# Kernel optimization log

Hardware: AMD Instinct MI355X
Metric: run time of the kernel (lower is better)

The kernel has to match this reference:

```python
import jax, jax.numpy as jnp
import numpy as np

H, W = 256, 256           # image_size
RES = 8                   # resolution
LAM_NOOBJ, LAM_ACCEL, LAM_VEL = 0.5, 1.0, 1.0
B_IMG = 129               # number of unique image indices in train_labels
K_BOX = 64                # boxes per image


def _make_labels():
    """Build label rows: [x, y, w, h, vx, vy, ax, ay, flag, img_idx] (int32).
    Cells are distinct within each image so scatter order is irrelevant."""
    rng = np.random.default_rng(0)
    rows = []
    for i in range(B_IMG):
        cells = rng.choice(H * W, K_BOX, replace=False)
        yc, xc = cells // W, cells % W
        x = xc * RES + rng.integers(0, RES, K_BOX)
        y = yc * RES + rng.integers(0, RES, K_BOX)
        wh = rng.integers(1, 32, (K_BOX, 2))
        traj = rng.integers(-10, 11, (K_BOX, 4))
        flag = np.full((K_BOX, 1), -1 if i % 16 == 0 else 0)
        img = np.full((K_BOX, 1), i)
        rows.append(np.concatenate([x[:, None], y[:, None], wh, traj, flag, img], axis=1))
    return np.concatenate(rows, 0).astype(np.int32)


def setup_inputs() -> dict:
    key = jax.random.key(0)
    output = jax.random.normal(key, (B_IMG - 1, 5, H, W), dtype=jnp.float32)
    train_labels = jnp.asarray(_make_labels())
    return {"output": output, "train_labels": train_labels, "num_images": B_IMG}


def _transform(train_labels, num_images):
    """Vectorized transform_LSTM_train: scatter per-box trajectories into dense grids."""
    Bm1 = num_images - 1
    img = train_labels[:, -1]
    # flag of each image's first row (constant per image in the data)
    first_flag = jax.ops.segment_max(train_labels[:, -2], img, num_segments=num_images)
    # loop starts at image 1; images whose flag == -1 are skipped
    valid = (img >= 1) & (first_flag[img] != -1)
    xc = train_labels[:, 0] // RES
    yc = train_labels[:, 1] // RES
    traj_v = train_labels[:, 4:8].astype(jnp.float32)
    # route invalid rows into an extra padding slot, then slice it off
    b = jnp.where(valid, img - 1, Bm1)
    traj = jnp.zeros((Bm1 + 1, 4, H, W), jnp.float32).at[b, :, yc, xc].set(traj_v)[:Bm1]
    o_m = jnp.zeros((Bm1 + 1, 1, H, W), jnp.float32).at[b, 0, yc, xc].set(1.0)[:Bm1]
    return traj, o_m


def _loss(output, traj, o_m):
    obj = o_m > 0           # [Bm1,1,H,W], broadcasts over channel dim
    noobj = ~obj
    pred_vel, pred_accel, pred_obj = output[:, :2], output[:, 2:4], output[:, -1:]
    n_obj = jnp.sum(obj).astype(jnp.float32)
    n_noobj = jnp.sum(noobj).astype(jnp.float32)
    # F.mse_loss over boolean-masked selections == masked sum / count
    noobj_loss = jnp.sum(jnp.where(noobj, (pred_obj - o_m) ** 2, 0.0)) / jnp.maximum(n_noobj, 1.0)
    vel_loss = jnp.sum(jnp.where(obj, (pred_vel - traj[:, :2]) ** 2, 0.0)) / jnp.maximum(2.0 * n_obj, 1.0)
    accel_loss = jnp.sum(jnp.where(obj, (pred_accel - traj[:, 2:]) ** 2, 0.0)) / jnp.maximum(2.0 * n_obj, 1.0)
    full = LAM_NOOBJ * noobj_loss + LAM_VEL * vel_loss + LAM_ACCEL * accel_loss
    return jnp.where(n_obj == 0, LAM_NOOBJ * noobj_loss, full)


def reference(output, train_labels, num_images):
    traj, o_m = _transform(train_labels, num_images)
    return _loss(output, traj, o_m)
```

## Files before the change

### kernel.cpp

```cpp
#include <hip/hip_runtime.h>
#include <limits.h>

constexpr int HW = 65536;
constexpr int RES_SHIFT = 3;
constexpr int NB = 1024;
constexpr int TPB = 256;

__device__ inline float wave_sum(float v) {
#pragma unroll
    for (int o = 32; o > 0; o >>= 1) v += __shfl_down(v, o, 64);
    return v;
}


__global__ void k_main(const float* __restrict__ out, int total4,
                       const int* __restrict__ labels, int n_rows,
                       float* __restrict__ partials_all,
                       float4* __restrict__ box_p) {
    const int nbox = (n_rows + TPB - 1) / TPB;
    const bool boxblk = blockIdx.x < nbox;

    bool bvalid = false;
    float o0 = 0, o1 = 0, o2 = 0, o3 = 0, o4 = 0;
    float vx = 0, vy = 0, ax = 0, ay = 0;
    if (boxblk) {
        int r = blockIdx.x * TPB + threadIdx.x;
        bool inb = r < n_rows;
        int flag = INT_MIN, img = -7, x = 0, y = 0;
        if (inb) {
            const int* L = labels + (size_t)r * 10;
            x = L[0]; y = L[1];
            vx = (float)L[4]; vy = (float)L[5];
            ax = (float)L[6]; ay = (float)L[7];
            flag = L[8]; img = L[9];
        }
        int f = flag;
#pragma unroll
        for (int o = 1; o < 64; o <<= 1) {
            int of = __shfl_xor(f, o, 64);
            int ok = __shfl_xor(img, o, 64);
            if (ok == img) f = max(f, of);
        }
        if (inb && img >= 1 && f != -1) {
            bvalid = true;
            int b = img - 1;
            int xc = x >> RES_SHIFT;
            int yc = y >> RES_SHIFT;
            size_t base = (((size_t)(b * 5)) << 16) + ((size_t)yc << 8) + (size_t)xc;
            o0 = out[base];
            o1 = out[base + HW];
            o2 = out[base + 2 * (size_t)HW];
            o3 = out[base + 3 * (size_t)HW];
            o4 = out[base + 4 * (size_t)HW];
        }
    }

    float acc = 0.0f;
    int stride = gridDim.x * blockDim.x;
    for (int idx = blockIdx.x * blockDim.x + threadIdx.x; idx < total4; idx += stride) {
        int b = idx >> 14;
        int w = idx & 16383;
        const float4 v = *reinterpret_cast<const float4*>(
            out + (((size_t)(b * 5 + 4)) << 16) + ((size_t)w << 2));
        acc += v.x * v.x + v.y * v.y + v.z * v.z + v.w * v.w;
    }
    __shared__ float s[4];
    acc = wave_sum(acc);
    if ((threadIdx.x & 63) == 0) s[threadIdx.x >> 6] = acc;
    __syncthreads();
    if (threadIdx.x == 0)
        partials_all[blockIdx.x] = s[0] + s[1] + s[2] + s[3];

    if (boxblk) {
        float vel = 0, acl = 0, osq = 0, cnt = 0;
        if (bvalid) {
            vel = (o0 - vx) * (o0 - vx) + (o1 - vy) * (o1 - vy);
            acl = (o2 - ax) * (o2 - ax) + (o3 - ay) * (o3 - ay);
            osq = o4 * o4;
            cnt = 1.0f;
        }
        osq = wave_sum(osq);
        vel = wave_sum(vel);
        acl = wave_sum(acl);
        cnt = wave_sum(cnt);
        __shared__ float sb[4][4];
        if ((threadIdx.x & 63) == 0) {
            int wv = threadIdx.x >> 6;
            sb[wv][0] = osq; sb[wv][1] = vel; sb[wv][2] = acl; sb[wv][3] = cnt;
        }
        __syncthreads();
        if (threadIdx.x == 0) {
            box_p[blockIdx.x] = make_float4(sb[0][0] + sb[1][0] + sb[2][0] + sb[3][0],
                                            sb[0][1] + sb[1][1] + sb[2][1] + sb[3][1],
                                            sb[0][2] + sb[1][2] + sb[2][2] + sb[3][2],
                                            sb[0][3] + sb[1][3] + sb[2][3] + sb[3][3]);
        }
    }
}

__global__ void k_final(const float* __restrict__ partials_all,
                        const float4* __restrict__ box_p,
                        int nb, int nbox, int Bm1, float* __restrict__ outp) {
    float all = 0.0f, osq = 0.0f, vel = 0.0f, acl = 0.0f, cnt = 0.0f;
    for (int i = threadIdx.x; i < nb; i += blockDim.x) all += partials_all[i];
    for (int i = threadIdx.x; i < nbox; i += blockDim.x) {
        float4 p = box_p[i];
        osq += p.x; vel += p.y; acl += p.z; cnt += p.w;
    }
    all = wave_sum(all); osq = wave_sum(osq); vel = wave_sum(vel);
    acl = wave_sum(acl); cnt = wave_sum(cnt);
    __shared__ float s[4][5];
    int lane = threadIdx.x & 63, wv = threadIdx.x >> 6;
    if (lane == 0) {
        s[wv][0] = all; s[wv][1] = osq; s[wv][2] = vel; s[wv][3] = acl; s[wv][4] = cnt;
    }
    __syncthreads();
    if (threadIdx.x == 0) {
        for (int i = 1; i < 4; ++i) {
            all += s[i][0]; osq += s[i][1]; vel += s[i][2]; acl += s[i][3]; cnt += s[i][4];
        }
        float n_obj = cnt;
        float total = (float)Bm1 * (float)HW;
        float n_noobj = total - n_obj;
        float noobj_loss = (all - osq) / fmaxf(n_noobj, 1.0f);
        float vel_loss = vel / fmaxf(2.0f * n_obj, 1.0f);
        float accel_loss = acl / fmaxf(2.0f * n_obj, 1.0f);
        float full = 0.5f * noobj_loss + vel_loss + accel_loss;
        outp[0] = (n_obj == 0.0f) ? (0.5f * noobj_loss) : full;
    }
}

extern "C" void kernel_launch(void* const* d_in, const int* in_sizes, int n_in,
                              void* d_out, int out_size, void* d_ws, size_t ws_size,
                              hipStream_t stream) {
    const float* output = (const float*)d_in[0];
    const int* labels = (const int*)d_in[1];

    int Bm1 = in_sizes[0] / (5 * HW);
    int n_rows = in_sizes[1] / 10;
    int total4 = Bm1 * (HW / 4);
    int nbox = (n_rows + TPB - 1) / TPB;

    char* ws = (char*)d_ws;
    float4* box_p = (float4*)ws;
    float* partials_all = (float*)(ws + 4096);

    k_main<<<NB, TPB, 0, stream>>>(output, total4, labels, n_rows,
                                   partials_all, box_p);
    k_final<<<1, 256, 0, stream>>>(partials_all, box_p, NB, nbox, Bm1, (float*)d_out);
}
```

Before: 15.99 us.

## Fuse final reduction into main kernel with last-block atomic and unroll loads

Removes the separate finalize kernel. Each block now bumps a global counter, and the last block to finish reads all partials and writes the loss. The main streaming loop issues eight float4 loads per thread before accumulating, to raise memory-level parallelism, and the grid is halved to 512 blocks. A memset is added to reset the counter on every launch, which costs an extra stream operation and relies on threadfence ordering being correct.

```diff
diff --git a/kernel.cpp b/kernel.cpp
--- a/kernel.cpp
+++ b/kernel.cpp
@@ -3,7 +3,7 @@
 
 constexpr int HW = 65536;
 constexpr int RES_SHIFT = 3;
-constexpr int NB = 1024;
+constexpr int NB = 512;
 constexpr int TPB = 256;
 
 __device__ inline float wave_sum(float v) {
@@ -12,13 +12,25 @@
     return v;
 }
 
+__device__ inline float sq4(const float4& v) {
+    return v.x * v.x + v.y * v.y + v.z * v.z + v.w * v.w;
+}
+
+__device__ inline float4 ld4(const float* __restrict__ out, int idx) {
+    int b = idx >> 14;
+    int w = idx & 16383;
+    return *reinterpret_cast<const float4*>(
+        out + (((size_t)(b * 5 + 4)) << 16) + ((size_t)w << 2));
+}
 
 __global__ void k_main(const float* __restrict__ out, int total4,
                        const int* __restrict__ labels, int n_rows,
                        float* __restrict__ partials_all,
-                       float4* __restrict__ box_p) {
+                       float4* __restrict__ box_p,
+                       unsigned* __restrict__ counter,
+                       int Bm1, float* __restrict__ outp) {
     const int nbox = (n_rows + TPB - 1) / TPB;
-    const bool boxblk = blockIdx.x < nbox;
+    const bool boxblk = blockIdx.x < (unsigned)nbox;
 
     bool bvalid = false;
     float o0 = 0, o1 = 0, o2 = 0, o3 = 0, o4 = 0;
@@ -56,14 +68,17 @@
     }
 
     float acc = 0.0f;
-    int stride = gridDim.x * blockDim.x;
-    for (int idx = blockIdx.x * blockDim.x + threadIdx.x; idx < total4; idx += stride) {
-        int b = idx >> 14;
-        int w = idx & 16383;
-        const float4 v = *reinterpret_cast<const float4*>(
-            out + (((size_t)(b * 5 + 4)) << 16) + ((size_t)w << 2));
-        acc += v.x * v.x + v.y * v.y + v.z * v.z + v.w * v.w;
+    const int S = gridDim.x * blockDim.x;
+    int idx = blockIdx.x * blockDim.x + threadIdx.x;
+    for (; idx + 7 * S < total4; idx += 8 * S) {
+        float4 v[8];
+#pragma unroll
+        for (int j = 0; j < 8; ++j) v[j] = ld4(out, idx + j * S);
+#pragma unroll
+        for (int j = 0; j < 8; ++j) acc += sq4(v[j]);
     }
+    for (; idx < total4; idx += S) acc += sq4(ld4(out, idx));
+
     __shared__ float s[4];
     acc = wave_sum(acc);
     if ((threadIdx.x & 63) == 0) s[threadIdx.x >> 6] = acc;
@@ -96,28 +111,35 @@
                                             sb[0][3] + sb[1][3] + sb[2][3] + sb[3][3]);
         }
     }
-}
 
-__global__ void k_final(const float* __restrict__ partials_all,
-                        const float4* __restrict__ box_p,
-                        int nb, int nbox, int Bm1, float* __restrict__ outp) {
+    __shared__ bool last;
+    if (threadIdx.x == 0) {
+        __threadfence();
+        unsigned old = atomicAdd(counter, 1u);
+        last = (old == gridDim.x - 1);
+    }
+    __syncthreads();
+    if (!last) return;
+    __threadfence();
+
     float all = 0.0f, osq = 0.0f, vel = 0.0f, acl = 0.0f, cnt = 0.0f;
-    for (int i = threadIdx.x; i < nb; i += blockDim.x) all += partials_all[i];
-    for (int i = threadIdx.x; i < nbox; i += blockDim.x) {
-        float4 p = box_p[i];
-        osq += p.x; vel += p.y; acl += p.z; cnt += p.w;
+    for (int i = threadIdx.x; i < NB; i += TPB) all += partials_all[i];
+    if (threadIdx.x < nbox) {
+        float4 p = box_p[threadIdx.x];
+        osq = p.x; vel = p.y; acl = p.z; cnt = p.w;
     }
     all = wave_sum(all); osq = wave_sum(osq); vel = wave_sum(vel);
     acl = wave_sum(acl); cnt = wave_sum(cnt);
-    __shared__ float s[4][5];
+    __shared__ float sf[4][5];
     int lane = threadIdx.x & 63, wv = threadIdx.x >> 6;
     if (lane == 0) {
-        s[wv][0] = all; s[wv][1] = osq; s[wv][2] = vel; s[wv][3] = acl; s[wv][4] = cnt;
+        sf[wv][0] = all; sf[wv][1] = osq; sf[wv][2] = vel; sf[wv][3] = acl; sf[wv][4] = cnt;
     }
     __syncthreads();
     if (threadIdx.x == 0) {
         for (int i = 1; i < 4; ++i) {
-            all += s[i][0]; osq += s[i][1]; vel += s[i][2]; acl += s[i][3]; cnt += s[i][4];
+            all += sf[i][0]; osq += sf[i][1]; vel += sf[i][2];
+            acl += sf[i][3]; cnt += sf[i][4];
         }
         float n_obj = cnt;
         float total = (float)Bm1 * (float)HW;
@@ -139,13 +161,14 @@
     int Bm1 = in_sizes[0] / (5 * HW);
     int n_rows = in_sizes[1] / 10;
     int total4 = Bm1 * (HW / 4);
-    int nbox = (n_rows + TPB - 1) / TPB;
 
     char* ws = (char*)d_ws;
-    float4* box_p = (float4*)ws;
-    float* partials_all = (float*)(ws + 4096);
+    unsigned* counter = (unsigned*)ws;
+    float* partials_all = (float*)(ws + 256);
+    float4* box_p = (float4*)(ws + 4096);
 
+    hipMemsetAsync(counter, 0, 4, stream);
     k_main<<<NB, TPB, 0, stream>>>(output, total4, labels, n_rows,
-                                   partials_all, box_p);
-    k_final<<<1, 256, 0, stream>>>(partials_all, box_p, NB, nbox, Bm1, (float*)d_out);
+                                   partials_all, box_p, counter,
+                                   Bm1, (float*)d_out);
 }
```

Measured after the change: 33.23 us. 2.08x slower.
